# Kernel tuning notes

Measured on AMD Instinct MI355X. Metric: run time of the kernel, lower is better.

The kernel has to match this reference:

```python
import jax, jax.numpy as jnp
import numpy as np

B, LQ, LK, D = 16, 2048, 2048, 256
NEG = -1e10


def setup_inputs() -> dict:
    key = jax.random.key(0)
    k1, k2, k3, k4, k5 = jax.random.split(key, 5)
    scale = 1.0 / np.sqrt(D)
    return {
        "x": jax.random.normal(k1, (B, LQ, D), dtype=jnp.float32),
        "y": jax.random.normal(k2, (B, LK, D), dtype=jnp.float32),
        "mask": jnp.zeros((B, LK), dtype=bool),  # True = padded key position
        "Wq": jax.random.normal(k3, (D, D), dtype=jnp.float32) * scale,
        "Wk": jax.random.normal(k4, (D, D), dtype=jnp.float32) * scale,
        "Wv": jax.random.normal(k5, (D, D), dtype=jnp.float32) * scale,
    }


def reference(x, y, mask, Wq, Wk, Wv):
    # nn.Linear: out = in @ W.T (no bias)
    q = jnp.einsum('bqd,ed->bqe', x, Wq)   # [B, LQ, D]
    k = jnp.einsum('bkd,ed->bke', y, Wk)   # [B, LK, D]
    v = jnp.einsum('bkd,ed->bke', y, Wv)   # [B, LK, D]
    # cdist (p=2) via GEMM expansion: ||q||^2 + ||k||^2 - 2 q.k
    qn = jnp.sum(q * q, axis=-1)                              # [B, LQ]
    kn = jnp.sum(k * k, axis=-1)                              # [B, LK]
    d2 = qn[:, :, None] + kn[:, None, :] - 2.0 * jnp.einsum('bqd,bkd->bqk', q, k)
    dist = jnp.sqrt(jnp.maximum(d2, 0.0))                     # [B, LQ, LK]
    scores = jnp.exp(-dist)
    # masked_fill: where original mask is True, set pre-softmax score to -1e10
    scores = jnp.where(mask[:, None, :], NEG, scores)
    attn = jax.nn.softmax(scores, axis=-1)                    # [B, LQ, LK]
    att_out = jnp.einsum('bqk,bkd->bqd', attn, v)             # [B, LQ, D]
    return (att_out, attn)
```

## Files before the change

kernel.cpp:

```cpp
#include <hip/hip_runtime.h>
#include <stdint.h>

#define B_   16
#define L_   2048
#define D_   256
#define NROW (B_*L_)

#define EPAD 40
#define TPAD 66

typedef __attribute__((ext_vector_type(8))) short s8v;
typedef __attribute__((ext_vector_type(4))) float f4v;

__device__ __forceinline__ unsigned short f2b(float f) {
    unsigned u = __builtin_bit_cast(unsigned, f);
    return (unsigned short)((u + 0x7fffu + ((u >> 16) & 1u)) >> 16);
}

__device__ __forceinline__ void gl16(const void* g, void* l) {
    __builtin_amdgcn_global_load_lds(
        (const __attribute__((address_space(1))) unsigned int*)g,
        (__attribute__((address_space(3))) unsigned int*)l, 16, 0, 0);
}

__global__ __launch_bounds__(256) void qkv_kernel(
    const float* __restrict__ x, const float* __restrict__ y,
    const float* __restrict__ Wq, const float* __restrict__ Wk, const float* __restrict__ Wv,
    unsigned short* __restrict__ Qb, unsigned short* __restrict__ Kb,
    unsigned short* __restrict__ Vt,
    float* __restrict__ qn, float* __restrict__ kn)
{
    __shared__ unsigned short Xs[64*256];
    __shared__ unsigned short Ws[64*256];
    __shared__ unsigned short Ts[64*TPAD];

    const int t    = threadIdx.x;
    const int r0   = blockIdx.x * 64;
    const int type = blockIdx.y;

    const float* X = type ? y : x;

    #pragma unroll
    for (int p = 0; p < 16; ++p) {
        int idx  = p*256 + t;
        int row  = idx >> 6;
        int half = idx & 1;
        int blk  = (idx & 63) >> 1;
        int c4   = blk*8 + half*4;
        float4 vx = *(const float4*)(X + (size_t)(r0+row)*D_ + c4);
        uint2 px;
        px.x = (unsigned)f2b(vx.x) | ((unsigned)f2b(vx.y) << 16);
        px.y = (unsigned)f2b(vx.z) | ((unsigned)f2b(vx.w) << 16);
        *(uint2*)(Xs + row*256 + (blk ^ (row & 15))*8 + half*4) = px;
    }

    const int w = t >> 6, lane = t & 63, q16 = lane & 15, quad = lane >> 4;
    const int m0 = w * 16;

    float p4[4] = {0.f, 0.f, 0.f, 0.f};
    const f4v z4 = {0.f, 0.f, 0.f, 0.f};

    for (int ct = 0; ct < 4; ++ct) {
        const int e0 = ct * 64;

        __syncthreads();
        {
            const float* W = type ? Wk : Wq;
            #pragma unroll
            for (int p = 0; p < 16; ++p) {
                int idx  = p*256 + t;
                int row  = idx >> 6;
                int half = idx & 1;
                int blk  = (idx & 63) >> 1;
                int c4   = blk*8 + half*4;
                float4 vw = *(const float4*)(W + (size_t)(e0+row)*D_ + c4);
                uint2 pw;
                pw.x = (unsigned)f2b(vw.x) | ((unsigned)f2b(vw.y) << 16);
                pw.y = (unsigned)f2b(vw.z) | ((unsigned)f2b(vw.w) << 16);
                *(uint2*)(Ws + row*256 + (blk ^ (row & 15))*8 + half*4) = pw;
            }
        }
        __syncthreads();

        f4v acc[4];
        #pragma unroll
        for (int n = 0; n < 4; ++n) acc[n] = z4;
        #pragma unroll
        for (int c = 0; c < 8; ++c) {
            s8v a = *(const s8v*)(Xs + (m0 + q16)*256 + (((c*4+quad) ^ q16)*8));
            #pragma unroll
            for (int n = 0; n < 4; ++n) {
                s8v bb = *(const s8v*)(Ws + (n*16 + q16)*256 + (((c*4+quad) ^ q16)*8));
                acc[n] = __builtin_amdgcn_mfma_f32_16x16x32_bf16(a, bb, acc[n], 0, 0, 0);
            }
        }
        {
            unsigned short* Out = type ? Kb : Qb;
            #pragma unroll
            for (int n = 0; n < 4; ++n)
                #pragma unroll
                for (int r = 0; r < 4; ++r) {
                    float v = acc[n][r];
                    p4[r] += v * v;
                    Out[(size_t)(r0 + m0 + quad*4 + r)*D_ + e0 + n*16 + q16] = f2b(v);
                }
        }

        if (type) {
            __syncthreads();
            #pragma unroll
            for (int p = 0; p < 16; ++p) {
                int idx  = p*256 + t;
                int row  = idx >> 6;
                int half = idx & 1;
                int blk  = (idx & 63) >> 1;
                int c4   = blk*8 + half*4;
                float4 vw = *(const float4*)(Wv + (size_t)(e0+row)*D_ + c4);
                uint2 pw;
                pw.x = (unsigned)f2b(vw.x) | ((unsigned)f2b(vw.y) << 16);
                pw.y = (unsigned)f2b(vw.z) | ((unsigned)f2b(vw.w) << 16);
                *(uint2*)(Ws + row*256 + (blk ^ (row & 15))*8 + half*4) = pw;
            }
            __syncthreads();

            f4v vacc[4];
            #pragma unroll
            for (int n = 0; n < 4; ++n) vacc[n] = z4;
            #pragma unroll
            for (int c = 0; c < 8; ++c) {
                s8v a = *(const s8v*)(Xs + (m0 + q16)*256 + (((c*4+quad) ^ q16)*8));
                #pragma unroll
                for (int n = 0; n < 4; ++n) {
                    s8v bb = *(const s8v*)(Ws + (n*16 + q16)*256 + (((c*4+quad) ^ q16)*8));
                    vacc[n] = __builtin_amdgcn_mfma_f32_16x16x32_bf16(a, bb, vacc[n], 0, 0, 0);
                }
            }
            #pragma unroll
            for (int n = 0; n < 4; ++n)
                #pragma unroll
                for (int r = 0; r < 4; ++r)
                    Ts[(m0 + quad*4 + r)*TPAD + n*16 + q16] = f2b(vacc[n][r]);
            __syncthreads();
            int j    = t >> 2;
            int kseg = t & 3;
            unsigned pk[8];
            #pragma unroll
            for (int i = 0; i < 8; ++i) {
                unsigned lo = Ts[(kseg*16 + 2*i    )*TPAD + j];
                unsigned hi = Ts[(kseg*16 + 2*i + 1)*TPAD + j];
                pk[i] = lo | (hi << 16);
            }
            int bb_ = r0 >> 11;
            int k0g = r0 & (L_ - 1);
            unsigned short* dst = Vt + (size_t)(bb_*D_ + e0 + j)*L_ + k0g + kseg*16;
            *(uint4*)dst       = make_uint4(pk[0], pk[1], pk[2], pk[3]);
            *((uint4*)dst + 1) = make_uint4(pk[4], pk[5], pk[6], pk[7]);
        }
    }

    {
        float* norm = type ? kn : qn;
        #pragma unroll
        for (int r = 0; r < 4; ++r) {
            float v = p4[r];
            v += __shfl_xor(v, 1, 16);
            v += __shfl_xor(v, 2, 16);
            v += __shfl_xor(v, 4, 16);
            v += __shfl_xor(v, 8, 16);
            if (q16 == 0) norm[r0 + m0 + quad*4 + r] = v;
        }
    }
}

__device__ __forceinline__ void stage_K(const unsigned short* Kb, unsigned short* ks,
                                        int bk, int k0, int w, int lane) {
    #pragma unroll
    for (int p = 0; p < 4; ++p) {
        int slot = p*256 + w*64 + lane;
        int row  = slot >> 5;
        int blk  = slot & 31;
        gl16(Kb + (size_t)(bk + k0 + row)*D_ + ((blk ^ (row & 15))*8),
             ks + (size_t)(p*256 + w*64)*8);
    }
}
__device__ __forceinline__ void stage_V(const unsigned short* Vt, unsigned short* vs,
                                        int bD, int k0, int w, int lane) {
    #pragma unroll
    for (int p = 0; p < 4; ++p) {
        int slot = p*256 + w*64 + lane;
        int d    = slot >> 2;
        int blk  = slot & 3;
        gl16(Vt + (size_t)(bD + d)*L_ + k0 + ((blk ^ ((d >> 1) & 3))*8),
             vs + (size_t)(p*256 + w*64)*8);
    }
}

__global__ __launch_bounds__(256) void rowsum_kernel(
    const unsigned short* __restrict__ Qb, const unsigned short* __restrict__ Kb,
    const float* __restrict__ qn, const float* __restrict__ kn,
    const unsigned char* __restrict__ mask,
    float* __restrict__ rowsum)
{
    __shared__ unsigned short Ks[2][32*256];

    const int t  = threadIdx.x;
    const int q0 = blockIdx.x * 64;
    const int b  = blockIdx.y;
    const int bk = b * L_;
    const int kbase = blockIdx.z * 1024;
    const int w = t >> 6, lane = t & 63, q16 = lane & 15, quad = lane >> 4;

    const int qrow = bk + q0 + w*16;
    s8v qa[8];
    float qnr[4];
    #pragma unroll
    for (int c = 0; c < 8; ++c)
        qa[c] = *(const s8v*)(Qb + (size_t)(qrow + q16)*D_ + c*32 + quad*8);
    #pragma unroll
    for (int r = 0; r < 4; ++r)
        qnr[r] = qn[qrow + quad*4 + r];

    float rs[4] = {0.f, 0.f, 0.f, 0.f};

    stage_K(Kb, Ks[0], bk, kbase, w, lane);
    for (int kt = 0; kt < 32; ++kt) {
        const int k0 = kbase + kt*32;
        const int cur = kt & 1;
        __syncthreads();
        if (kt < 31) stage_K(Kb, Ks[cur ^ 1], bk, k0 + 32, w, lane);

        float kcv[2]; int mkv[2];
        #pragma unroll
        for (int n = 0; n < 2; ++n) {
            kcv[n] = kn[bk + k0 + n*16 + q16];
            mkv[n] = mask[bk + k0 + n*16 + q16];
        }
        #pragma unroll
        for (int n = 0; n < 2; ++n) {
            f4v s = {0.f, 0.f, 0.f, 0.f};
            #pragma unroll
            for (int c = 0; c < 8; ++c) {
                s8v bb = *(const s8v*)(Ks[cur] + (n*16 + q16)*256 + (((c*4+quad) ^ q16)*8));
                s = __builtin_amdgcn_mfma_f32_16x16x32_bf16(qa[c], bb, s, 0, 0, 0);
            }
            #pragma unroll
            for (int r = 0; r < 4; ++r) {
                float d2 = qnr[r] + kcv[n] - 2.0f * s[r];
                float dist = sqrtf(fmaxf(d2, 0.f));
                rs[r] += mkv[n] ? 0.f : __expf(__expf(-dist));
            }
        }
    }

    #pragma unroll
    for (int r = 0; r < 4; ++r) {
        float v = rs[r];
        v += __shfl_xor(v, 1, 16);
        v += __shfl_xor(v, 2, 16);
        v += __shfl_xor(v, 4, 16);
        v += __shfl_xor(v, 8, 16);
        if (q16 == 0) atomicAdd(rowsum + qrow + quad*4 + r, v);
    }
}

__global__ __launch_bounds__(256) void attnout_kernel(
    const unsigned short* __restrict__ Qb, const unsigned short* __restrict__ Kb,
    const unsigned short* __restrict__ Vt,
    const float* __restrict__ qn, const float* __restrict__ kn,
    const float* __restrict__ rowsum,
    const unsigned char* __restrict__ mask,
    float* __restrict__ attn_out, float* __restrict__ att_out)
{
    __shared__ unsigned short Ks[2][32*256];
    __shared__ unsigned short Vs[2][256*32];
    __shared__ unsigned short Es[4][16*EPAD];

    const int t  = threadIdx.x;
    const int q0 = blockIdx.x * 64;
    const int b  = blockIdx.y;
    const int bk = b * L_;
    const int bD = b * D_;
    const int w = t >> 6, lane = t & 63, q16 = lane & 15, quad = lane >> 4;

    const int qrow = bk + q0 + w*16;
    s8v qa[8];
    float qnr[4], inv[4];
    #pragma unroll
    for (int c = 0; c < 8; ++c)
        qa[c] = *(const s8v*)(Qb + (size_t)(qrow + q16)*D_ + c*32 + quad*8);
    #pragma unroll
    for (int r = 0; r < 4; ++r) {
        qnr[r] = qn[qrow + quad*4 + r];
        inv[r] = 1.0f / rowsum[qrow + quad*4 + r];
    }

    const f4v z4 = {0.f, 0.f, 0.f, 0.f};
    f4v O[16];
    #pragma unroll
    for (int n = 0; n < 16; ++n) O[n] = z4;

    stage_K(Kb, Ks[0], bk, 0, w, lane);
    stage_V(Vt, Vs[0], bD, 0, w, lane);
    for (int kt = 0; kt < 64; ++kt) {
        const int k0 = kt * 32;
        const int cur = kt & 1;
        __syncthreads();
        if (kt < 63) {
            stage_K(Kb, Ks[cur ^ 1], bk, k0 + 32, w, lane);
            stage_V(Vt, Vs[cur ^ 1], bD, k0 + 32, w, lane);
        }

        float kcv[2]; int mkv[2];
        #pragma unroll
        for (int n = 0; n < 2; ++n) {
            kcv[n] = kn[bk + k0 + n*16 + q16];
            mkv[n] = mask[bk + k0 + n*16 + q16];
        }

        #pragma unroll
        for (int n = 0; n < 2; ++n) {
            f4v s = {0.f, 0.f, 0.f, 0.f};
            #pragma unroll
            for (int c = 0; c < 8; ++c) {
                s8v bb = *(const s8v*)(Ks[cur] + (n*16 + q16)*256 + (((c*4+quad) ^ q16)*8));
                s = __builtin_amdgcn_mfma_f32_16x16x32_bf16(qa[c], bb, s, 0, 0, 0);
            }
            #pragma unroll
            for (int r = 0; r < 4; ++r) {
                float d2 = qnr[r] + kcv[n] - 2.0f * s[r];
                float dist = sqrtf(fmaxf(d2, 0.f));
                float E = mkv[n] ? 0.f : __expf(__expf(-dist));
                float av = E * inv[r];
                attn_out[(size_t)(qrow + quad*4 + r)*L_ + k0 + n*16 + q16] = av;
                Es[w][(quad*4 + r)*EPAD + n*16 + q16] =
                    (unsigned short)(__builtin_bit_cast(unsigned, av) >> 16);
            }
        }
        s8v af = *(const s8v*)(&Es[w][q16*EPAD + quad*8]);
        #pragma unroll
        for (int n = 0; n < 16; ++n) {
            s8v vb = *(const s8v*)(Vs[cur] + (n*16 + q16)*32 +
                                   ((quad ^ ((q16 >> 1) & 3))*8));
            O[n] = __builtin_amdgcn_mfma_f32_16x16x32_bf16(af, vb, O[n], 0, 0, 0);
        }
    }

    #pragma unroll
    for (int n = 0; n < 16; ++n)
        #pragma unroll
        for (int r = 0; r < 4; ++r)
            att_out[(size_t)(qrow + quad*4 + r)*D_ + n*16 + q16] = O[n][r];
}

extern "C" void kernel_launch(void* const* d_in, const int* in_sizes, int n_in,
                              void* d_out, int out_size, void* d_ws, size_t ws_size,
                              hipStream_t stream) {
    (void)in_sizes; (void)n_in; (void)out_size; (void)ws_size;
    const float* x  = (const float*)d_in[0];
    const float* y  = (const float*)d_in[1];
    const unsigned char* mask = (const unsigned char*)d_in[2];
    const float* Wq = (const float*)d_in[3];
    const float* Wk = (const float*)d_in[4];
    const float* Wv = (const float*)d_in[5];

    char* ws = (char*)d_ws;
    unsigned short* Qb = (unsigned short*)ws;
    unsigned short* Kb = Qb + (size_t)NROW * D_;
    unsigned short* Vt = Kb + (size_t)NROW * D_;
    float* qn     = (float*)(ws + 3 * (size_t)NROW * D_ * 2);
    float* kn     = qn + NROW;
    float* rowsum = kn + NROW;

    float* att_out = (float*)d_out;
    float* attn    = att_out + (size_t)NROW * D_;

    hipMemsetAsync(rowsum, 0, (size_t)NROW * sizeof(float), stream);
    qkv_kernel<<<dim3(512, 2), 256, 0, stream>>>(x, y, Wq, Wk, Wv,
                                                 Qb, Kb, Vt, qn, kn);
    rowsum_kernel<<<dim3(32, 16, 2), 256, 0, stream>>>(Qb, Kb, qn, kn, mask, rowsum);
    attnout_kernel<<<dim3(32, 16), 256, 0, stream>>>(Qb, Kb, Vt, qn, kn, rowsum,
                                                     mask, attn, att_out);
}
```

Measured before the change: 612.8 us.

## Fuse rowsum into PV kernel and split attention-weight write into separate kernel

The row-sum reduction moves into the P·V kernel. That kernel accumulates unnormalized exp scores, multiplies by V, and normalizes the output at the end. A new kernel recomputes the scores and writes the normalized attention matrix, split over two key halves for more blocks. This removes the memset and the atomic rowsum pass, and takes the large attn store out of the MFMA-heavy PV loop. In exchange, the P·V product is now computed from unnormalized bf16 weights, which may change rounding.

```diff
diff --git a/kernel.cpp b/kernel.cpp
--- a/kernel.cpp
+++ b/kernel.cpp
@@ -195,81 +195,12 @@
     }
 }
 
-__global__ __launch_bounds__(256) void rowsum_kernel(
-    const unsigned short* __restrict__ Qb, const unsigned short* __restrict__ Kb,
-    const float* __restrict__ qn, const float* __restrict__ kn,
-    const unsigned char* __restrict__ mask,
-    float* __restrict__ rowsum)
-{
-    __shared__ unsigned short Ks[2][32*256];
-
-    const int t  = threadIdx.x;
-    const int q0 = blockIdx.x * 64;
-    const int b  = blockIdx.y;
-    const int bk = b * L_;
-    const int kbase = blockIdx.z * 1024;
-    const int w = t >> 6, lane = t & 63, q16 = lane & 15, quad = lane >> 4;
-
-    const int qrow = bk + q0 + w*16;
-    s8v qa[8];
-    float qnr[4];
-    #pragma unroll
-    for (int c = 0; c < 8; ++c)
-        qa[c] = *(const s8v*)(Qb + (size_t)(qrow + q16)*D_ + c*32 + quad*8);
-    #pragma unroll
-    for (int r = 0; r < 4; ++r)
-        qnr[r] = qn[qrow + quad*4 + r];
-
-    float rs[4] = {0.f, 0.f, 0.f, 0.f};
-
-    stage_K(Kb, Ks[0], bk, kbase, w, lane);
-    for (int kt = 0; kt < 32; ++kt) {
-        const int k0 = kbase + kt*32;
-        const int cur = kt & 1;
-        __syncthreads();
-        if (kt < 31) stage_K(Kb, Ks[cur ^ 1], bk, k0 + 32, w, lane);
-
-        float kcv[2]; int mkv[2];
-        #pragma unroll
-        for (int n = 0; n < 2; ++n) {
-            kcv[n] = kn[bk + k0 + n*16 + q16];
-            mkv[n] = mask[bk + k0 + n*16 + q16];
-        }
-        #pragma unroll
-        for (int n = 0; n < 2; ++n) {
-            f4v s = {0.f, 0.f, 0.f, 0.f};
-            #pragma unroll
-            for (int c = 0; c < 8; ++c) {
-                s8v bb = *(const s8v*)(Ks[cur] + (n*16 + q16)*256 + (((c*4+quad) ^ q16)*8));
-                s = __builtin_amdgcn_mfma_f32_16x16x32_bf16(qa[c], bb, s, 0, 0, 0);
-            }
-            #pragma unroll
-            for (int r = 0; r < 4; ++r) {
-                float d2 = qnr[r] + kcv[n] - 2.0f * s[r];
-                float dist = sqrtf(fmaxf(d2, 0.f));
-                rs[r] += mkv[n] ? 0.f : __expf(__expf(-dist));
-            }
-        }
-    }
-
-    #pragma unroll
-    for (int r = 0; r < 4; ++r) {
-        float v = rs[r];
-        v += __shfl_xor(v, 1, 16);
-        v += __shfl_xor(v, 2, 16);
-        v += __shfl_xor(v, 4, 16);
-        v += __shfl_xor(v, 8, 16);
-        if (q16 == 0) atomicAdd(rowsum + qrow + quad*4 + r, v);
-    }
-}
-
-__global__ __launch_bounds__(256) void attnout_kernel(
+__global__ __launch_bounds__(256) void attnpv_kernel(
     const unsigned short* __restrict__ Qb, const unsigned short* __restrict__ Kb,
     const unsigned short* __restrict__ Vt,
     const float* __restrict__ qn, const float* __restrict__ kn,
-    const float* __restrict__ rowsum,
     const unsigned char* __restrict__ mask,
-    float* __restrict__ attn_out, float* __restrict__ att_out)
+    float* __restrict__ rowsum, float* __restrict__ att_out)
 {
     __shared__ unsigned short Ks[2][32*256];
     __shared__ unsigned short Vs[2][256*32];
@@ -284,16 +215,15 @@
 
     const int qrow = bk + q0 + w*16;
     s8v qa[8];
-    float qnr[4], inv[4];
+    float qnr[4];
     #pragma unroll
     for (int c = 0; c < 8; ++c)
         qa[c] = *(const s8v*)(Qb + (size_t)(qrow + q16)*D_ + c*32 + quad*8);
     #pragma unroll
-    for (int r = 0; r < 4; ++r) {
+    for (int r = 0; r < 4; ++r)
         qnr[r] = qn[qrow + quad*4 + r];
-        inv[r] = 1.0f / rowsum[qrow + quad*4 + r];
-    }
-
+
+    float rs[4] = {0.f, 0.f, 0.f, 0.f};
     const f4v z4 = {0.f, 0.f, 0.f, 0.f};
     f4v O[16];
     #pragma unroll
@@ -330,10 +260,9 @@
                 float d2 = qnr[r] + kcv[n] - 2.0f * s[r];
                 float dist = sqrtf(fmaxf(d2, 0.f));
                 float E = mkv[n] ? 0.f : __expf(__expf(-dist));
-                float av = E * inv[r];
-                attn_out[(size_t)(qrow + quad*4 + r)*L_ + k0 + n*16 + q16] = av;
+                rs[r] += E;
                 Es[w][(quad*4 + r)*EPAD + n*16 + q16] =
-                    (unsigned short)(__builtin_bit_cast(unsigned, av) >> 16);
+                    (unsigned short)(__builtin_bit_cast(unsigned, E) >> 16);
             }
         }
         s8v af = *(const s8v*)(&Es[w][q16*EPAD + quad*8]);
@@ -345,11 +274,83 @@
         }
     }
 
+    float inv[4];
+    #pragma unroll
+    for (int r = 0; r < 4; ++r) {
+        float v = rs[r];
+        v += __shfl_xor(v, 1, 16);
+        v += __shfl_xor(v, 2, 16);
+        v += __shfl_xor(v, 4, 16);
+        v += __shfl_xor(v, 8, 16);
+        if (q16 == 0) rowsum[qrow + quad*4 + r] = v;
+        inv[r] = 1.0f / v;
+    }
+
     #pragma unroll
     for (int n = 0; n < 16; ++n)
         #pragma unroll
         for (int r = 0; r < 4; ++r)
-            att_out[(size_t)(qrow + quad*4 + r)*D_ + n*16 + q16] = O[n][r];
+            att_out[(size_t)(qrow + quad*4 + r)*D_ + n*16 + q16] = O[n][r] * inv[r];
+}
+
+__global__ __launch_bounds__(256) void attnw_kernel(
+    const unsigned short* __restrict__ Qb, const unsigned short* __restrict__ Kb,
+    const float* __restrict__ qn, const float* __restrict__ kn,
+    const float* __restrict__ rowsum,
+    const unsigned char* __restrict__ mask,
+    float* __restrict__ attn_out)
+{
+    __shared__ unsigned short Ks[2][32*256];
+
+    const int t  = threadIdx.x;
+    const int q0 = blockIdx.x * 64;
+    const int b  = blockIdx.y;
+    const int bk = b * L_;
+    const int kbase = blockIdx.z * 1024;
+    const int w = t >> 6, lane = t & 63, q16 = lane & 15, quad = lane >> 4;
+
+    const int qrow = bk + q0 + w*16;
+    s8v qa[8];
+    float qnr[4], inv[4];
+    #pragma unroll
+    for (int c = 0; c < 8; ++c)
+        qa[c] = *(const s8v*)(Qb + (size_t)(qrow + q16)*D_ + c*32 + quad*8);
+    #pragma unroll
+    for (int r = 0; r < 4; ++r) {
+        qnr[r] = qn[qrow + quad*4 + r];
+        inv[r] = 1.0f / rowsum[qrow + quad*4 + r];
+    }
+
+    stage_K(Kb, Ks[0], bk, kbase, w, lane);
+    for (int kt = 0; kt < 32; ++kt) {
+        const int k0 = kbase + kt*32;
+        const int cur = kt & 1;
+        __syncthreads();
+        if (kt < 31) stage_K(Kb, Ks[cur ^ 1], bk, k0 + 32, w, lane);
+
+        float kcv[2]; int mkv[2];
+        #pragma unroll
+        for (int n = 0; n < 2; ++n) {
+            kcv[n] = kn[bk + k0 + n*16 + q16];
+            mkv[n] = mask[bk + k0 + n*16 + q16];
+        }
+        #pragma unroll
+        for (int n = 0; n < 2; ++n) {
+            f4v s = {0.f, 0.f, 0.f, 0.f};
+            #pragma unroll
+            for (int c = 0; c < 8; ++c) {
+                s8v bb = *(const s8v*)(Ks[cur] + (n*16 + q16)*256 + (((c*4+quad) ^ q16)*8));
+                s = __builtin_amdgcn_mfma_f32_16x16x32_bf16(qa[c], bb, s, 0, 0, 0);
+            }
+            #pragma unroll
+            for (int r = 0; r < 4; ++r) {
+                float d2 = qnr[r] + kcv[n] - 2.0f * s[r];
+                float dist = sqrtf(fmaxf(d2, 0.f));
+                float E = mkv[n] ? 0.f : __expf(__expf(-dist));
+                attn_out[(size_t)(qrow + quad*4 + r)*L_ + k0 + n*16 + q16] = E * inv[r];
+            }
+        }
+    }
 }
 
 extern "C" void kernel_launch(void* const* d_in, const int* in_sizes, int n_in,
@@ -374,10 +375,10 @@
     float* att_out = (float*)d_out;
     float* attn    = att_out + (size_t)NROW * D_;
 
-    hipMemsetAsync(rowsum, 0, (size_t)NROW * sizeof(float), stream);
     qkv_kernel<<<dim3(512, 2), 256, 0, stream>>>(x, y, Wq, Wk, Wv,
                                                  Qb, Kb, Vt, qn, kn);
-    rowsum_kernel<<<dim3(32, 16, 2), 256, 0, stream>>>(Qb, Kb, qn, kn, mask, rowsum);
-    attnout_kernel<<<dim3(32, 16), 256, 0, stream>>>(Qb, Kb, Vt, qn, kn, rowsum,
-                                                     mask, attn, att_out);
-}
+    attnpv_kernel<<<dim3(32, 16), 256, 0, stream>>>(Qb, Kb, Vt, qn, kn, mask,
+                                                    rowsum, att_out);
+    attnw_kernel<<<dim3(32, 16, 2), 256, 0, stream>>>(Qb, Kb, qn, kn, rowsum,
+                                                      mask, attn);
+}
```

Measured after the change: 636.1 us. 3.8% more time.
